# Kernel tuning notes

Hardware: AMD Instinct MI355X
Metric: run time of the kernel (lower is better)

Reference implementation:

```python
import jax, jax.numpy as jnp
import numpy as np

HBLK = 16  # hadamard / nvfp4 block size
FP4_LEVELS = jnp.array([0.0, 0.5, 1.0, 1.5, 2.0, 3.0, 4.0, 6.0], dtype=jnp.float32)
FP4_MIDS = jnp.array([0.25, 0.75, 1.25, 1.75, 2.5, 3.5, 5.0], dtype=jnp.float32)


def _hadamard(n):
    H = np.array([[1.0]])
    while H.shape[0] < n:
        H = np.block([[H, H], [H, -H]])
    return jnp.asarray(H / np.sqrt(n), dtype=jnp.float32)  # orthonormal

H16 = _hadamard(HBLK)


def rht_forward(x, signs):
    # x: [M, K], K % 16 == 0 (no padding needed). Random sign diag then block Hadamard.
    M, K = x.shape
    xb = x.reshape(M, K // HBLK, HBLK)
    return ((xb * signs) @ H16).reshape(M, K)


def q_emulate(x):
    # NVFP4 quantize->dequantize along last dim: blocks of 16, E4M3 block scale = amax/6,
    # round-to-nearest onto E2M1 grid {0,.5,1,1.5,2,3,4,6} (signed).
    M, K = x.shape
    xb = x.reshape(M, K // HBLK, HBLK)
    amax = jnp.max(jnp.abs(xb), axis=-1, keepdims=True)
    scale = (amax / 6.0).astype(jnp.float8_e4m3fn).astype(x.dtype)
    safe = jnp.where(scale == 0, 1.0, scale)
    a = jnp.clip(jnp.abs(xb) / safe, 0.0, 6.0)
    q = FP4_LEVELS[jnp.searchsorted(FP4_MIDS, a)]
    return (jnp.sign(xb) * q * scale).reshape(M, K)


def setup_inputs() -> dict:
    key = jax.random.key(0)
    kx, kw, kb, ks1, ks2 = jax.random.split(key, 5)
    IN, OUT = 4096, 4096
    x = jax.random.normal(kx, (4, 2048, IN), dtype=jnp.float32)
    weight = jax.random.normal(kw, (OUT, IN), dtype=jnp.float32) / np.sqrt(IN)
    bound = 1.0 / np.sqrt(IN)
    bias = jax.random.uniform(kb, (OUT,), dtype=jnp.float32, minval=-bound, maxval=bound)
    signs_in = jnp.where(jax.random.bernoulli(ks1, 0.5, (HBLK,)), 1.0, -1.0).astype(jnp.float32)
    signs_grad = jnp.where(jax.random.bernoulli(ks2, 0.5, (HBLK,)), 1.0, -1.0).astype(jnp.float32)
    return {"x": x, "weight": weight, "bias": bias, "signs_in": signs_in, "signs_grad": signs_grad}


def reference(x, weight, bias, signs_in, signs_grad):
    # signs_grad only used in backward (kept for interface parity).
    x_flat = x.reshape(-1, x.shape[-1])
    x_q = q_emulate(rht_forward(x_flat, signs_in))
    w_q = q_emulate(rht_forward(weight, signs_in))
    y = x_q @ w_q.T + bias
    return y.reshape(*x.shape[:-1], weight.shape[0])
```

## Files before the change

### kernel.cpp

```cpp
#include <hip/hip_runtime.h>
#include <stdint.h>


typedef __bf16 bf16x8 __attribute__((ext_vector_type(8)));
typedef float f32x4 __attribute__((ext_vector_type(4)));


__device__ __forceinline__ float e4m3_rt(float x) {
    unsigned int u = __float_as_uint(x);
    int ex = (int)((u >> 23) & 0xffu) - 127;
    if (ex < -6) ex = -6;
    float qs = __uint_as_float((unsigned)(127 + 3 - ex) << 23);
    float qi = __uint_as_float((unsigned)(127 + ex - 3) << 23);
    return rintf(x * qs) * qi;
}

__device__ __forceinline__ float quant1(float tv, float safe, float scale) {
    float aa = fminf(fabsf(tv) / safe, 6.0f);
    float q = aa > 2.5f ? (aa > 5.0f ? 6.0f : (aa > 3.5f ? 4.0f : 3.0f))
                        : (aa > 1.25f ? (aa > 1.75f ? 2.0f : 1.5f)
                                      : (aa > 0.75f ? 1.0f
                                         : (aa > 0.25f ? 0.5f : 0.0f)));
    return copysignf(q * scale, tv);
}

__device__ __forceinline__ unsigned pack2(float lo, float hi) {
    return (__float_as_uint(lo) >> 16) | (__float_as_uint(hi) & 0xFFFF0000u);
}

__global__ __launch_bounds__(256) void quant_rht_kernel(
    const float* __restrict__ X, const float* __restrict__ signs,
    uint16_t* __restrict__ Q, int ngroups)
{
    int gid = blockIdx.x * 256 + threadIdx.x;
    if (gid >= ngroups) return;

    const float4* p = (const float4*)(X + (size_t)gid * 16);
    float4 v0 = p[0], v1 = p[1], v2 = p[2], v3 = p[3];
    const float4* sp = (const float4*)signs;
    float4 s0 = sp[0], s1 = sp[1], s2 = sp[2], s3 = sp[3];

    float t0 = v0.x * s0.x, t1 = v0.y * s0.y, t2 = v0.z * s0.z, t3 = v0.w * s0.w;
    float t4 = v1.x * s1.x, t5 = v1.y * s1.y, t6 = v1.z * s1.z, t7 = v1.w * s1.w;
    float t8 = v2.x * s2.x, t9 = v2.y * s2.y, t10 = v2.z * s2.z, t11 = v2.w * s2.w;
    float t12 = v3.x * s3.x, t13 = v3.y * s3.y, t14 = v3.z * s3.z, t15 = v3.w * s3.w;

#define BT(a, b) { float _s = (a) + (b), _d = (a) - (b); (a) = _s; (b) = _d; }
    BT(t0,t1)  BT(t2,t3)  BT(t4,t5)   BT(t6,t7)
    BT(t8,t9)  BT(t10,t11) BT(t12,t13) BT(t14,t15)
    BT(t0,t2)  BT(t1,t3)  BT(t4,t6)   BT(t5,t7)
    BT(t8,t10) BT(t9,t11) BT(t12,t14) BT(t13,t15)
    BT(t0,t4)  BT(t1,t5)  BT(t2,t6)   BT(t3,t7)
    BT(t8,t12) BT(t9,t13) BT(t10,t14) BT(t11,t15)
    BT(t0,t8)  BT(t1,t9)  BT(t2,t10)  BT(t3,t11)
    BT(t4,t12) BT(t5,t13) BT(t6,t14)  BT(t7,t15)
#undef BT

    t0 *= 0.25f;  t1 *= 0.25f;  t2 *= 0.25f;  t3 *= 0.25f;
    t4 *= 0.25f;  t5 *= 0.25f;  t6 *= 0.25f;  t7 *= 0.25f;
    t8 *= 0.25f;  t9 *= 0.25f;  t10 *= 0.25f; t11 *= 0.25f;
    t12 *= 0.25f; t13 *= 0.25f; t14 *= 0.25f; t15 *= 0.25f;

    float amax = fmaxf(
        fmaxf(fmaxf(fmaxf(fabsf(t0), fabsf(t1)), fmaxf(fabsf(t2), fabsf(t3))),
              fmaxf(fmaxf(fabsf(t4), fabsf(t5)), fmaxf(fabsf(t6), fabsf(t7)))),
        fmaxf(fmaxf(fmaxf(fabsf(t8), fabsf(t9)), fmaxf(fabsf(t10), fabsf(t11))),
              fmaxf(fmaxf(fabsf(t12), fabsf(t13)), fmaxf(fabsf(t14), fabsf(t15)))));

    float scale = e4m3_rt(amax / 6.0f);
    float safe = (scale == 0.0f) ? 1.0f : scale;

    unsigned w0 = pack2(quant1(t0, safe, scale),  quant1(t1, safe, scale));
    unsigned w1 = pack2(quant1(t2, safe, scale),  quant1(t3, safe, scale));
    unsigned w2 = pack2(quant1(t4, safe, scale),  quant1(t5, safe, scale));
    unsigned w3 = pack2(quant1(t6, safe, scale),  quant1(t7, safe, scale));
    unsigned w4 = pack2(quant1(t8, safe, scale),  quant1(t9, safe, scale));
    unsigned w5 = pack2(quant1(t10, safe, scale), quant1(t11, safe, scale));
    unsigned w6 = pack2(quant1(t12, safe, scale), quant1(t13, safe, scale));
    unsigned w7 = pack2(quant1(t14, safe, scale), quant1(t15, safe, scale));

    uint4* q4 = (uint4*)(Q + (size_t)gid * 16);
    q4[0] = make_uint4(w0, w1, w2, w3);
    q4[1] = make_uint4(w4, w5, w6, w7);
}


#define BM 256
#define BN 256

__global__ __launch_bounds__(512, 2) void gemm_bt_bias(
    const uint16_t* __restrict__ A,
    const uint16_t* __restrict__ B,
    const float* __restrict__ bias,
    float* __restrict__ C,
    int M, int N, int K)
{
    __shared__ uint4 sh[8][1024];

    const int tid  = threadIdx.x;
    const int lane = tid & 63;
    const int wave = tid >> 6;
    const int wm = wave >> 2, wn = wave & 3;
    const int lm = lane & 15, g4 = lane >> 4;
    const int bn = blockIdx.x, bm = blockIdx.y;

    const int NT  = K >> 6;
    const int NHT = NT << 2;

    const int p0 = tid, p1 = 512 + tid;
    const int c0 = p0 ^ ((p0 >> 3) & 7);
    const int c1 = p1 ^ ((p1 >> 3) & 7);
    const uint16_t* asrc0 = A + (size_t)(bm * BM + (c0 >> 2)) * K + (c0 & 3) * 8;
    const uint16_t* asrc1 = A + (size_t)(bm * BM + (c1 >> 2)) * K + (c1 & 3) * 8;
    const uint16_t* bsrc0 = B + (size_t)(bn * BN + (c0 >> 2)) * K + (c0 & 3) * 8;
    const uint16_t* bsrc1 = B + (size_t)(bn * BN + (c1 >> 2)) * K + (c1 & 3) * 8;
    char* ldsd0 = (char*)&sh[0][0] + p0 * 16;
    char* ldsd1 = (char*)&sh[0][0] + p1 * 16;

    int aPos[8], bPos[4];
#pragma unroll
    for (int f = 0; f < 8; ++f) {
        int c = (wm * 128 + f * 16 + lm) * 4 + g4;
        aPos[f] = c ^ ((c >> 3) & 7);
    }
#pragma unroll
    for (int f = 0; f < 4; ++f) {
        int c = (wn * 64 + f * 16 + lm) * 4 + g4;
        bPos[f] = c ^ ((c >> 3) & 7);
    }

    f32x4 acc[8][4];
#pragma unroll
    for (int i = 0; i < 8; ++i)
#pragma unroll
        for (int j = 0; j < 4; ++j) acc[i][j] = (f32x4){0.f, 0.f, 0.f, 0.f};

    bf16x8 a0[4], a1[4], b0[4], b1[4];

#define STAGE(jj) do {                                                        \
    int _j = (jj);                                                            \
    int _koff = (_j < NHT) ? (((_j >> 2) << 6) | (((_j >> 1) & 1) << 5)) : 0; \
    int _sb = (_j & 7) << 14;                                                 \
    const uint16_t* _s0 = (_j & 1) ? bsrc0 : asrc0;                           \
    const uint16_t* _s1 = (_j & 1) ? bsrc1 : asrc1;                           \
    __builtin_amdgcn_global_load_lds(                                         \
        (const __attribute__((address_space(1))) unsigned int*)(_s0 + _koff), \
        (__attribute__((address_space(3))) unsigned int*)(ldsd0 + _sb),       \
        16, 0, 0);                                                            \
    __builtin_amdgcn_global_load_lds(                                         \
        (const __attribute__((address_space(1))) unsigned int*)(_s1 + _koff), \
        (__attribute__((address_space(3))) unsigned int*)(ldsd1 + _sb),       \
        16, 0, 0);                                                            \
} while (0)

#define WIN(ARH, CA, CB, NA, NSA, NRH, LOADB, NB, NSB, SJ, GATE) do {         \
    _Pragma("unroll")                                                         \
    for (int _i = 0; _i < 4; ++_i)                                            \
        NA[_i] = __builtin_bit_cast(bf16x8, sh[NSA][aPos[4*(NRH) + _i]]);     \
    if (LOADB) {                                                              \
        _Pragma("unroll")                                                     \
        for (int _jj = 0; _jj < 4; ++_jj)                                     \
            NB[_jj] = __builtin_bit_cast(bf16x8, sh[NSB][bPos[_jj]]);         \
    }                                                                         \
    STAGE(hb + (SJ));                                                         \
    if (GATE) asm volatile("s_waitcnt vmcnt(4)" ::: "memory");                \
    __builtin_amdgcn_sched_barrier(0);                                        \
    __builtin_amdgcn_s_setprio(1);                                            \
    _Pragma("unroll")                                                         \
    for (int _i = 0; _i < 4; ++_i)                                            \
        _Pragma("unroll")                                                     \
        for (int _jj = 0; _jj < 4; ++_jj)                                     \
            acc[4*(ARH) + _i][_jj] = __builtin_amdgcn_mfma_f32_16x16x32_bf16( \
                CA[_i], CB[_jj], acc[4*(ARH) + _i][_jj], 0, 0, 0);            \
    __builtin_amdgcn_s_setprio(0);                                            \
    __builtin_amdgcn_sched_barrier(0);                                        \
    __builtin_amdgcn_s_barrier();                                             \
} while (0)

    STAGE(0); STAGE(1); STAGE(2); STAGE(3); STAGE(4); STAGE(5);
    asm volatile("s_waitcnt vmcnt(8)" ::: "memory");
    __builtin_amdgcn_s_barrier();
#pragma unroll
    for (int i = 0; i < 4; ++i)
        a1[i] = __builtin_bit_cast(bf16x8, sh[0][aPos[i]]);
#pragma unroll
    for (int j = 0; j < 4; ++j)
        b0[j] = __builtin_bit_cast(bf16x8, sh[1][bPos[j]]);

    const int NT2 = NT >> 1;
    for (int it2 = 0; it2 < NT2; ++it2) {
        const int hb = it2 << 3;
        WIN(0, a1, b0, a0, 0, 1, 0, b1, 0,  6, 1);
        WIN(1, a0, b0, a1, 2, 0, 1, b1, 3,  7, 0);
        WIN(0, a1, b1, a0, 2, 1, 0, b0, 0,  8, 1);
        WIN(1, a0, b1, a1, 4, 0, 1, b0, 5,  9, 0);
        WIN(0, a1, b0, a0, 4, 1, 0, b1, 0, 10, 1);
        WIN(1, a0, b0, a1, 6, 0, 1, b1, 7, 11, 0);
        WIN(0, a1, b1, a0, 6, 1, 0, b0, 0, 12, 1);
        WIN(1, a0, b1, a1, 0, 0, 1, b0, 1, 13, 0);
    }
    asm volatile("s_waitcnt vmcnt(0) lgkmcnt(0)" ::: "memory");

#undef WIN
#undef STAGE

#pragma unroll
    for (int j = 0; j < 4; ++j) {
        int col = bn * BN + wn * 64 + j * 16 + lm;
        float bj = bias[col];
#pragma unroll
        for (int i = 0; i < 8; ++i) {
            int row0 = bm * BM + wm * 128 + i * 16 + g4 * 4;
#pragma unroll
            for (int r = 0; r < 4; ++r) {
                C[(size_t)(row0 + r) * (size_t)N + col] = acc[i][j][r] + bj;
            }
        }
    }
}


extern "C" void kernel_launch(void* const* d_in, const int* in_sizes, int n_in,
                              void* d_out, int out_size, void* d_ws, size_t ws_size,
                              hipStream_t stream)
{
    const float* x        = (const float*)d_in[0];
    const float* w        = (const float*)d_in[1];
    const float* bias     = (const float*)d_in[2];
    const float* signs_in = (const float*)d_in[3];

    const int OUT = in_sizes[2];
    const int IN  = in_sizes[1] / OUT;
    const int M   = in_sizes[0] / IN;

    uint16_t* xq = (uint16_t*)d_ws;
    uint16_t* wq = xq + (size_t)M * (size_t)IN;
    (void)ws_size; (void)n_in; (void)out_size;

    int ngx = (int)((size_t)M * IN / 16);
    int ngw = (int)((size_t)OUT * IN / 16);
    quant_rht_kernel<<<(ngx + 255) / 256, 256, 0, stream>>>(x, signs_in, xq, ngx);
    quant_rht_kernel<<<(ngw + 255) / 256, 256, 0, stream>>>(w, signs_in, wq, ngw);

    dim3 grid(OUT / BN, M / BM);
    gemm_bt_bias<<<grid, 512, 0, stream>>>(xq, wq, bias, (float*)d_out, M, OUT, IN);
}
```

Before: 487.7 us.

## Issue MFMAs before LDS reads and staging; precompute quantization thresholds

The GEMM window macro now issues its MFMA block first, then the LDS fragment reads for the next window and the async global-to-LDS stage. The sched_barrier between the loads and the MFMAs is gone, and the vmcnt gate is relaxed from 4 to 6 outstanding loads. The aim is to overlap memory traffic with matrix math instead of serializing them. Separately, the quantize kernel multiplies the midpoint thresholds by the scale once per group, replacing a per-element divide. The reordered pipeline changes the wait-count accounting and carries a risk of LDS read/write hazards if the gate no longer covers the buffer being read.

New measurement: 473.4 us. 2.9% less time.

```diff
diff --git a/kernel.cpp b/kernel.cpp
--- a/kernel.cpp
+++ b/kernel.cpp
@@ -13,15 +13,6 @@
     float qs = __uint_as_float((unsigned)(127 + 3 - ex) << 23);
     float qi = __uint_as_float((unsigned)(127 + ex - 3) << 23);
     return rintf(x * qs) * qi;
-}
-
-__device__ __forceinline__ float quant1(float tv, float safe, float scale) {
-    float aa = fminf(fabsf(tv) / safe, 6.0f);
-    float q = aa > 2.5f ? (aa > 5.0f ? 6.0f : (aa > 3.5f ? 4.0f : 3.0f))
-                        : (aa > 1.25f ? (aa > 1.75f ? 2.0f : 1.5f)
-                                      : (aa > 0.75f ? 1.0f
-                                         : (aa > 0.25f ? 0.5f : 0.0f)));
-    return copysignf(q * scale, tv);
 }
 
 __device__ __forceinline__ unsigned pack2(float lo, float hi) {
@@ -70,14 +61,26 @@
     float scale = e4m3_rt(amax / 6.0f);
     float safe = (scale == 0.0f) ? 1.0f : scale;
 
-    unsigned w0 = pack2(quant1(t0, safe, scale),  quant1(t1, safe, scale));
-    unsigned w1 = pack2(quant1(t2, safe, scale),  quant1(t3, safe, scale));
-    unsigned w2 = pack2(quant1(t4, safe, scale),  quant1(t5, safe, scale));
-    unsigned w3 = pack2(quant1(t6, safe, scale),  quant1(t7, safe, scale));
-    unsigned w4 = pack2(quant1(t8, safe, scale),  quant1(t9, safe, scale));
-    unsigned w5 = pack2(quant1(t10, safe, scale), quant1(t11, safe, scale));
-    unsigned w6 = pack2(quant1(t12, safe, scale), quant1(t13, safe, scale));
-    unsigned w7 = pack2(quant1(t14, safe, scale), quant1(t15, safe, scale));
+    float m1 = 0.25f * safe, m2 = 0.75f * safe, m3 = 1.25f * safe,
+          m4 = 1.75f * safe, m5 = 2.5f * safe,  m6 = 3.5f * safe,
+          m7 = 5.0f * safe;
+
+#define Q1(tv) ({                                                              \
+    float _a = fabsf(tv);                                                      \
+    float _q = _a > m5 ? (_a > m7 ? 6.0f : (_a > m6 ? 4.0f : 3.0f))            \
+                       : (_a > m3 ? (_a > m4 ? 2.0f : 1.5f)                    \
+                                  : (_a > m2 ? 1.0f : (_a > m1 ? 0.5f : 0.0f)));\
+    copysignf(_q * scale, (tv)); })
+
+    unsigned w0 = pack2(Q1(t0),  Q1(t1));
+    unsigned w1 = pack2(Q1(t2),  Q1(t3));
+    unsigned w2 = pack2(Q1(t4),  Q1(t5));
+    unsigned w3 = pack2(Q1(t6),  Q1(t7));
+    unsigned w4 = pack2(Q1(t8),  Q1(t9));
+    unsigned w5 = pack2(Q1(t10), Q1(t11));
+    unsigned w6 = pack2(Q1(t12), Q1(t13));
+    unsigned w7 = pack2(Q1(t14), Q1(t15));
+#undef Q1
 
     uint4* q4 = (uint4*)(Q + (size_t)gid * 16);
     q4[0] = make_uint4(w0, w1, w2, w3);
@@ -154,6 +157,14 @@
 } while (0)
 
 #define WIN(ARH, CA, CB, NA, NSA, NRH, LOADB, NB, NSB, SJ, GATE) do {         \
+    __builtin_amdgcn_s_setprio(1);                                            \
+    _Pragma("unroll")                                                         \
+    for (int _i = 0; _i < 4; ++_i)                                            \
+        _Pragma("unroll")                                                     \
+        for (int _jj = 0; _jj < 4; ++_jj)                                     \
+            acc[4*(ARH) + _i][_jj] = __builtin_amdgcn_mfma_f32_16x16x32_bf16( \
+                CA[_i], CB[_jj], acc[4*(ARH) + _i][_jj], 0, 0, 0);            \
+    __builtin_amdgcn_s_setprio(0);                                            \
     _Pragma("unroll")                                                         \
     for (int _i = 0; _i < 4; ++_i)                                            \
         NA[_i] = __builtin_bit_cast(bf16x8, sh[NSA][aPos[4*(NRH) + _i]]);     \
@@ -163,16 +174,7 @@
             NB[_jj] = __builtin_bit_cast(bf16x8, sh[NSB][bPos[_jj]]);         \
     }                                                                         \
     STAGE(hb + (SJ));                                                         \
-    if (GATE) asm volatile("s_waitcnt vmcnt(4)" ::: "memory");                \
-    __builtin_amdgcn_sched_barrier(0);                                        \
-    __builtin_amdgcn_s_setprio(1);                                            \
-    _Pragma("unroll")                                                         \
-    for (int _i = 0; _i < 4; ++_i)                                            \
-        _Pragma("unroll")                                                     \
-        for (int _jj = 0; _jj < 4; ++_jj)                                     \
-            acc[4*(ARH) + _i][_jj] = __builtin_amdgcn_mfma_f32_16x16x32_bf16( \
-                CA[_i], CB[_jj], acc[4*(ARH) + _i][_jj], 0, 0, 0);            \
-    __builtin_amdgcn_s_setprio(0);                                            \
+    if (GATE) asm volatile("s_waitcnt vmcnt(6)" ::: "memory");                \
     __builtin_amdgcn_sched_barrier(0);                                        \
     __builtin_amdgcn_s_barrier();                                             \
 } while (0)
```
